# Optimization experiments

Measured on AMD Instinct MI355X. Metric: run time of the kernel, lower is better.

## Reference

```python
import jax, jax.numpy as jnp
import numpy as np

WINDOW = 256   # init kwarg window_size
CAUSAL = False # init kwarg causal


def setup_inputs() -> dict:
    key = jax.random.key(0)
    k1, k2, k3 = jax.random.split(key, 3)
    shape = (2, 16, 4096, 64)  # (batch, heads, seq_len, head_dim); seq_len % WINDOW == 0
    return {
        "query": jax.random.normal(k1, shape, dtype=jnp.float32),
        "key": jax.random.normal(k2, shape, dtype=jnp.float32),
        "value": jax.random.normal(k3, shape, dtype=jnp.float32),
    }


def _neighbor_blocks(x, nb, W):
    # x: [B,H,S,D] -> [B,H,nb,3W,D] where block n holds key blocks n-1,n,n+1 (zero padded at ends)
    B, H, S, D = x.shape
    xb = x.reshape(B, H, nb, W, D)
    xp = jnp.pad(xb, ((0, 0), (0, 0), (1, 1), (0, 0), (0, 0)))
    return jnp.concatenate([xp[:, :, j:j + nb] for j in range(3)], axis=3)


def _swa(query, key, value, window, causal):
    B, H, S, D = query.shape
    W = window
    nb = S // W
    scale = jnp.float32(1.0 / np.sqrt(D))
    qb = query.reshape(B, H, nb, W, D)
    kb = _neighbor_blocks(key, nb, W)    # [B,H,nb,3W,D]
    vb = _neighbor_blocks(value, nb, W)  # [B,H,nb,3W,D]

    # band mask: query global pos qi = n*W + q, key global pos ki = n*W + (k - W)
    qpos = jnp.arange(W)[:, None]              # [W,1]
    kpos = jnp.arange(3 * W)[None, :] - W      # [1,3W] relative block offset
    diff = kpos - qpos                         # [W,3W] == ki - qi
    ki = jnp.arange(nb)[:, None, None] * W + kpos[None]  # [nb,1,3W]
    valid = (ki >= 0) & (ki < S)
    if causal:
        band = (diff >= -W) & (diff <= 0)
    else:
        band = jnp.abs(diff) <= W
    mask = valid & band[None]                  # [nb,W,3W]

    scores = jnp.einsum('bhnqd,bhnkd->bhnqk', qb, kb) * scale  # [B,H,nb,W,3W]
    scores = jnp.where(mask, scores, -jnp.inf)
    attn = jax.nn.softmax(scores, axis=-1)
    out = jnp.einsum('bhnqk,bhnkd->bhnqd', attn, vb)
    return out.reshape(B, H, S, D)


def reference(query, key, value):
    return _swa(query, key, value, WINDOW, CAUSAL)
```

## Files before the change

kernel.cpp:

```cpp
#include <hip/hip_runtime.h>
#include <hip/hip_bf16.h>

typedef __attribute__((ext_vector_type(4)))  float f32x4;
typedef __attribute__((ext_vector_type(16))) float f32x16;
typedef __attribute__((ext_vector_type(8)))  short bf16x8;
typedef __attribute__((ext_vector_type(4)))  unsigned u32x4;

#define S_LEN 4096
#define HEAD_D 64
#define WIN 256
#define QBLK 128
#define KVBLK 64
#define KSTR 72
#define VSTR 72
#define QSCALE 0.18033688f

#define KBYTES (KVBLK * KSTR * 2)
#define VBYTES (HEAD_D * VSTR * 2)
#define KHALF  (KBYTES / 2)
#define VHALF  (VBYTES / 2)
#define LPAR_OFF (2 * KBYTES + 2 * VBYTES)
#define SMEM_BYTES (LPAR_OFF + 2 * 4 * 32 * 4)

static __device__ __forceinline__ unsigned cvt2(float lo, float hi) {
  unsigned r;
  asm("v_cvt_pk_bf16_f32 %0, %1, %2" : "=v"(r) : "v"(lo), "v"(hi));
  return r;
}

#define PUB_BARRIER() do {                              \
    __builtin_amdgcn_sched_barrier(0);                  \
    asm volatile("s_waitcnt lgkmcnt(0)" ::: "memory");  \
    __builtin_amdgcn_s_barrier();                       \
    __builtin_amdgcn_sched_barrier(0);                  \
  } while (0)

__global__ __launch_bounds__(512, 4)
void swa_fwd(const float* __restrict__ Q, const float* __restrict__ K,
             const float* __restrict__ V, float* __restrict__ O) {
  __shared__ __attribute__((aligned(16))) char smem[SMEM_BYTES];

  const int tid  = threadIdx.x;
  const int widx = tid >> 6;
  const int lane = tid & 63;
  const int hi   = lane >> 5;
  const int c    = lane & 31;
  const int qg   = widx & 3;
  const int kh   = widx >> 2;
  const int kho  = kh * 32;

  const int pb  = blockIdx.x;
  const int bh  = (pb & 7) * 4 + ((pb >> 3) >> 5);
  const int qb  = (pb >> 3) & 31;
  const int bq0 = qb * QBLK;
  const int q0w = bq0 + qg * 32;

  const size_t base = (size_t)bh * S_LEN * HEAD_D;
  const float* Qp = Q + base;
  const float* Kp = K + base;
  const float* Vp = V + base;
  float*       Op = O + base;

  const f32x16 Z16 = {0.f,0.f,0.f,0.f,0.f,0.f,0.f,0.f,0.f,0.f,0.f,0.f,0.f,0.f,0.f,0.f};

  bf16x8 aq[4];
  {
    const float* qr = Qp + (size_t)(q0w + c) * HEAD_D + hi * 8;
    #pragma unroll
    for (int ch = 0; ch < 4; ++ch) {
      f32x4 x0 = *(const f32x4*)(qr + ch * 16);
      f32x4 x1 = *(const f32x4*)(qr + ch * 16 + 4);
      u32x4 au;
      au[0] = cvt2(x0[0] * QSCALE, x0[1] * QSCALE);
      au[1] = cvt2(x0[2] * QSCALE, x0[3] * QSCALE);
      au[2] = cvt2(x1[0] * QSCALE, x1[1] * QSCALE);
      au[3] = cvt2(x1[2] * QSCALE, x1[3] * QSCALE);
      aq[ch] = __builtin_bit_cast(bf16x8, au);
    }
  }

  f32x16 acc0 = Z16, acc1 = Z16;
  float lsA = 0.f, lsB = 0.f;

  const int lo   = max(0, bq0 - WIN);
  const int khiB = min(S_LEN, bq0 + QBLK + WIN);
  const int nt   = (khiB - lo) >> 6;

  const int krow  = tid >> 3;
  const int kc8   = (tid & 7) << 3;
  const int key2  = (tid & 31) << 1;
  const int key2p = (key2 & ~12) | ((key2 & 4) << 1) | ((key2 & 8) >> 1);
  const int vd4   = (tid >> 5) << 2;

  short* const ksh = (short*)smem;
  short* const vsh = (short*)(smem + 2 * KBYTES);
  const short* const krd = ksh + (kho + c) * KSTR + hi * 8;
  const short* const vrd = vsh + c * VSTR + kho + hi * 8;
  short* const kwr = ksh + krow * KSTR + kc8;
  short* const vwr = vsh + vd4 * VSTR + key2p;

  unsigned koff = (unsigned)(lo + krow) * HEAD_D + kc8;
  unsigned voff = (unsigned)(lo + key2) * HEAD_D + vd4;

  f32x4 ka0, ka1, va0, va1;
  #define LOAD_TILE() do {                          \
    ka0 = *(const f32x4*)(Kp + koff);               \
    ka1 = *(const f32x4*)(Kp + koff + 4);           \
    va0 = *(const f32x4*)(Vp + voff);               \
    va1 = *(const f32x4*)(Vp + voff + HEAD_D);      \
    koff += KVBLK * HEAD_D;                         \
    voff += KVBLK * HEAD_D;                         \
  } while (0)

  #define STAGE_TO(BUF) do {                                        \
    u32x4 kw;                                                       \
    kw[0] = cvt2(ka0[0], ka0[1]);                                   \
    kw[1] = cvt2(ka0[2], ka0[3]);                                   \
    kw[2] = cvt2(ka1[0], ka1[1]);                                   \
    kw[3] = cvt2(ka1[2], ka1[3]);                                   \
    *(u32x4*)&kwr[(BUF) * KHALF] = kw;                              \
    _Pragma("unroll")                                               \
    for (int j = 0; j < 4; ++j)                                     \
      *(unsigned*)&vwr[(BUF) * VHALF + j * VSTR] = cvt2(va0[j], va1[j]); \
  } while (0)

  #define TILE_BODY(T, BUF) do {                                              \
    const int kv0_ = lo + ((T) << 6);                                         \
    f32x16 s = Z16;                                                           \
    __builtin_amdgcn_s_setprio(1);                                            \
    _Pragma("unroll")                                                         \
    for (int ch = 0; ch < 4; ++ch) {                                          \
      bf16x8 akf = *(const bf16x8*)&krd[(BUF) * KHALF + ch * 16];             \
      s = __builtin_amdgcn_mfma_f32_32x32x16_bf16(akf, aq[ch], s, 0, 0, 0);   \
    }                                                                         \
    __builtin_amdgcn_s_setprio(0);                                            \
    const int rel_ = kv0_ + kho - q0w;                                        \
    if (rel_ >= -224 && rel_ <= 224) {                                        \
      _Pragma("unroll")                                                       \
      for (int g = 0; g < 16; g += 2) {                                       \
        const float p0 = exp2f(s[g]);                                         \
        const float p1 = exp2f(s[g + 1]);                                     \
        s[g] = p0; s[g + 1] = p1; lsA += p0; lsB += p1;                       \
      }                                                                       \
    } else {                                                                  \
      const int bm_ = rel_ + 4 * hi - c + WIN;                                \
      _Pragma("unroll")                                                       \
      for (int g = 0; g < 16; ++g) {                                          \
        const int ro_ = (g & 3) + 8 * (g >> 2);                               \
        const float p = ((unsigned)(bm_ + ro_) <= 2u * WIN) ? exp2f(s[g]) : 0.f; \
        s[g] = p; if (g & 1) lsB += p; else lsA += p;                         \
      }                                                                       \
    }                                                                         \
    __builtin_amdgcn_s_setprio(1);                                            \
    _Pragma("unroll")                                                         \
    for (int kt = 0; kt < 2; ++kt) {                                          \
      u32x4 pau;                                                              \
      _Pragma("unroll")                                                       \
      for (int p2 = 0; p2 < 4; ++p2)                                          \
        pau[p2] = cvt2(s[kt * 8 + 2 * p2], s[kt * 8 + 2 * p2 + 1]);           \
      const bf16x8 pa = __builtin_bit_cast(bf16x8, pau);                      \
      bf16x8 bv0 = *(const bf16x8*)&vrd[(BUF) * VHALF + kt * 16];             \
      acc0 = __builtin_amdgcn_mfma_f32_32x32x16_bf16(pa, bv0, acc0, 0, 0, 0); \
      bf16x8 bv1 = *(const bf16x8*)&vrd[(BUF) * VHALF + kt * 16 + 32 * VSTR]; \
      acc1 = __builtin_amdgcn_mfma_f32_32x32x16_bf16(pa, bv1, acc1, 0, 0, 0); \
    }                                                                         \
    __builtin_amdgcn_s_setprio(0);                                            \
    if ((T) + 1 < nt) {                                                       \
      STAGE_TO((BUF) ^ 1);                                                    \
      if ((T) + 2 < nt) LOAD_TILE();                                          \
      PUB_BARRIER();                                                          \
    }                                                                         \
  } while (0)

  LOAD_TILE();
  STAGE_TO(0);
  LOAD_TILE();
  PUB_BARRIER();

  for (int t = 0; t < nt; t += 2) {
    TILE_BODY(t, 0);
    TILE_BODY(t + 1, 1);
  }

  float lsum = lsA + lsB;
  lsum += __shfl_xor(lsum, 32);
  __syncthreads();
  float* o_mrg = (float*)smem;
  float* l_par = (float*)(smem + LPAR_OFF);
  if (hi == 0) l_par[(kh * 4 + qg) * 32 + c] = lsum;
  if (kh == 0) {
    #pragma unroll
    for (int g = 0; g < 16; ++g) {
      const int qrow = (g & 3) + 8 * (g >> 2) + 4 * hi;
      o_mrg[(qg * 32 + qrow) * HEAD_D + c]      = acc0[g];
      o_mrg[(qg * 32 + qrow) * HEAD_D + 32 + c] = acc1[g];
    }
  }
  __syncthreads();
  if (kh == 1) {
    if (hi == 0) l_par[qg * 32 + c] = 1.0f / (l_par[qg * 32 + c] + l_par[(4 + qg) * 32 + c]);
    __asm__ volatile("s_waitcnt lgkmcnt(0)" ::: "memory");
    __builtin_amdgcn_sched_barrier(0);
    #pragma unroll
    for (int g = 0; g < 16; ++g) {
      const int qrow = (g & 3) + 8 * (g >> 2) + 4 * hi;
      const float iv = l_par[qg * 32 + qrow];
      float* orow = Op + (size_t)(q0w + qrow) * HEAD_D;
      orow[c]      = (o_mrg[(qg * 32 + qrow) * HEAD_D + c]      + acc0[g]) * iv;
      orow[32 + c] = (o_mrg[(qg * 32 + qrow) * HEAD_D + 32 + c] + acc1[g]) * iv;
    }
  }
}

extern "C" void kernel_launch(void* const* d_in, const int* in_sizes, int n_in,
                              void* d_out, int out_size, void* d_ws, size_t ws_size,
                              hipStream_t stream) {
  const float* q = (const float*)d_in[0];
  const float* k = (const float*)d_in[1];
  const float* v = (const float*)d_in[2];
  float* o = (float*)d_out;
  const int blocks = 2 * 16 * (S_LEN / QBLK);
  swa_fwd<<<dim3(blocks), dim3(512), 0, stream>>>(q, k, v, o);
}
```

Before: 51.25 us.

## Give each wave two query sets to reuse K/V fragments, halving block size

Workgroups shrink from 8 waves to 4. Each wave now handles two 32-row query sets that share every K and V fragment read from LDS, so each fragment feeds twice as many MFMAs. K and V global loads are split and issued between phases of the tile body, replacing the single next-tile prefetch, and exp2f becomes the raw hardware exp2 builtin. The cost is roughly double the accumulator and score registers per wave, fewer waves per block to hide latency, and a changed launch-bounds occupancy target.

```diff
diff --git a/kernel.cpp b/kernel.cpp
--- a/kernel.cpp
+++ b/kernel.cpp
@@ -20,7 +20,7 @@
 #define KHALF  (KBYTES / 2)
 #define VHALF  (VBYTES / 2)
 #define LPAR_OFF (2 * KBYTES + 2 * VBYTES)
-#define SMEM_BYTES (LPAR_OFF + 2 * 4 * 32 * 4)
+#define SMEM_BYTES (LPAR_OFF + 2 * 2 * 2 * 32 * 4)
 
 static __device__ __forceinline__ unsigned cvt2(float lo, float hi) {
   unsigned r;
@@ -35,25 +35,25 @@
     __builtin_amdgcn_sched_barrier(0);                  \
   } while (0)
 
-__global__ __launch_bounds__(512, 4)
+__global__ __launch_bounds__(256, 3)
 void swa_fwd(const float* __restrict__ Q, const float* __restrict__ K,
              const float* __restrict__ V, float* __restrict__ O) {
   __shared__ __attribute__((aligned(16))) char smem[SMEM_BYTES];
 
-  const int tid  = threadIdx.x;
-  const int widx = tid >> 6;
-  const int lane = tid & 63;
-  const int hi   = lane >> 5;
-  const int c    = lane & 31;
-  const int qg   = widx & 3;
-  const int kh   = widx >> 2;
-  const int kho  = kh * 32;
+  const int tid   = threadIdx.x;
+  const int widx  = tid >> 6;
+  const int lane  = tid & 63;
+  const int hi    = lane >> 5;
+  const int c     = lane & 31;
+  const int kh    = widx & 1;
+  const int qpair = widx >> 1;
+  const int kho   = kh * 32;
 
   const int pb  = blockIdx.x;
   const int bh  = (pb & 7) * 4 + ((pb >> 3) >> 5);
   const int qb  = (pb >> 3) & 31;
   const int bq0 = qb * QBLK;
-  const int q0w = bq0 + qg * 32;
+  const int q0  = bq0 + qpair * 64;
 
   const size_t base = (size_t)bh * S_LEN * HEAD_D;
   const float* Qp = Q + base;
@@ -63,9 +63,10 @@
 
   const f32x16 Z16 = {0.f,0.f,0.f,0.f,0.f,0.f,0.f,0.f,0.f,0.f,0.f,0.f,0.f,0.f,0.f,0.f};
 
-  bf16x8 aq[4];
-  {
-    const float* qr = Qp + (size_t)(q0w + c) * HEAD_D + hi * 8;
+  bf16x8 aqA[4], aqB[4];
+  #pragma unroll
+  for (int set = 0; set < 2; ++set) {
+    const float* qr = Qp + (size_t)(q0 + set * 32 + c) * HEAD_D + hi * 8;
     #pragma unroll
     for (int ch = 0; ch < 4; ++ch) {
       f32x4 x0 = *(const f32x4*)(qr + ch * 16);
@@ -75,106 +76,131 @@
       au[1] = cvt2(x0[2] * QSCALE, x0[3] * QSCALE);
       au[2] = cvt2(x1[0] * QSCALE, x1[1] * QSCALE);
       au[3] = cvt2(x1[2] * QSCALE, x1[3] * QSCALE);
-      aq[ch] = __builtin_bit_cast(bf16x8, au);
-    }
-  }
-
-  f32x16 acc0 = Z16, acc1 = Z16;
-  float lsA = 0.f, lsB = 0.f;
+      if (set == 0) aqA[ch] = __builtin_bit_cast(bf16x8, au);
+      else          aqB[ch] = __builtin_bit_cast(bf16x8, au);
+    }
+  }
+
+  f32x16 accA0 = Z16, accA1 = Z16, accB0 = Z16, accB1 = Z16;
+  float lsA0 = 0.f, lsA1 = 0.f, lsB0 = 0.f, lsB1 = 0.f;
 
   const int lo   = max(0, bq0 - WIN);
   const int khiB = min(S_LEN, bq0 + QBLK + WIN);
   const int nt   = (khiB - lo) >> 6;
 
-  const int krow  = tid >> 3;
-  const int kc8   = (tid & 7) << 3;
+  const int krow  = tid >> 2;
+  const int kc16  = (tid & 3) << 4;
   const int key2  = (tid & 31) << 1;
   const int key2p = (key2 & ~12) | ((key2 & 4) << 1) | ((key2 & 8) >> 1);
-  const int vd4   = (tid >> 5) << 2;
+  const int vd8   = (tid >> 5) << 3;
 
   short* const ksh = (short*)smem;
   short* const vsh = (short*)(smem + 2 * KBYTES);
   const short* const krd = ksh + (kho + c) * KSTR + hi * 8;
   const short* const vrd = vsh + c * VSTR + kho + hi * 8;
-  short* const kwr = ksh + krow * KSTR + kc8;
-  short* const vwr = vsh + vd4 * VSTR + key2p;
-
-  unsigned koff = (unsigned)(lo + krow) * HEAD_D + kc8;
-  unsigned voff = (unsigned)(lo + key2) * HEAD_D + vd4;
-
-  f32x4 ka0, ka1, va0, va1;
-  #define LOAD_TILE() do {                          \
-    ka0 = *(const f32x4*)(Kp + koff);               \
-    ka1 = *(const f32x4*)(Kp + koff + 4);           \
-    va0 = *(const f32x4*)(Vp + voff);               \
-    va1 = *(const f32x4*)(Vp + voff + HEAD_D);      \
-    koff += KVBLK * HEAD_D;                         \
-    voff += KVBLK * HEAD_D;                         \
-  } while (0)
-
+  short* const kwr = ksh + krow * KSTR + kc16;
+  short* const vwr = vsh + vd8 * VSTR + key2p;
+
+  unsigned koff = (unsigned)(lo + krow) * HEAD_D + kc16;
+  unsigned voff = (unsigned)(lo + key2) * HEAD_D + vd8;
+
+  f32x4 k0, k1, k2, k3;
+  f32x4 v00, v01, v10, v11;
+  #define LOAD_K() do {                         \
+    k0 = *(const f32x4*)(Kp + koff);            \
+    k1 = *(const f32x4*)(Kp + koff + 4);        \
+    k2 = *(const f32x4*)(Kp + koff + 8);        \
+    k3 = *(const f32x4*)(Kp + koff + 12);       \
+    koff += KVBLK * HEAD_D;                     \
+  } while (0)
+  #define LOAD_V() do {                         \
+    v00 = *(const f32x4*)(Vp + voff);           \
+    v01 = *(const f32x4*)(Vp + voff + 4);       \
+    v10 = *(const f32x4*)(Vp + voff + HEAD_D);  \
+    v11 = *(const f32x4*)(Vp + voff + HEAD_D + 4); \
+    voff += KVBLK * HEAD_D;                     \
+  } while (0)
   #define STAGE_TO(BUF) do {                                        \
     u32x4 kw;                                                       \
-    kw[0] = cvt2(ka0[0], ka0[1]);                                   \
-    kw[1] = cvt2(ka0[2], ka0[3]);                                   \
-    kw[2] = cvt2(ka1[0], ka1[1]);                                   \
-    kw[3] = cvt2(ka1[2], ka1[3]);                                   \
+    kw[0] = cvt2(k0[0], k0[1]);  kw[1] = cvt2(k0[2], k0[3]);        \
+    kw[2] = cvt2(k1[0], k1[1]);  kw[3] = cvt2(k1[2], k1[3]);        \
     *(u32x4*)&kwr[(BUF) * KHALF] = kw;                              \
+    kw[0] = cvt2(k2[0], k2[1]);  kw[1] = cvt2(k2[2], k2[3]);        \
+    kw[2] = cvt2(k3[0], k3[1]);  kw[3] = cvt2(k3[2], k3[3]);        \
+    *(u32x4*)&kwr[(BUF) * KHALF + 8] = kw;                          \
     _Pragma("unroll")                                               \
     for (int j = 0; j < 4; ++j)                                     \
-      *(unsigned*)&vwr[(BUF) * VHALF + j * VSTR] = cvt2(va0[j], va1[j]); \
-  } while (0)
-
-  #define TILE_BODY(T, BUF) do {                                              \
-    const int kv0_ = lo + ((T) << 6);                                         \
-    f32x16 s = Z16;                                                           \
-    __builtin_amdgcn_s_setprio(1);                                            \
-    _Pragma("unroll")                                                         \
-    for (int ch = 0; ch < 4; ++ch) {                                          \
-      bf16x8 akf = *(const bf16x8*)&krd[(BUF) * KHALF + ch * 16];             \
-      s = __builtin_amdgcn_mfma_f32_32x32x16_bf16(akf, aq[ch], s, 0, 0, 0);   \
-    }                                                                         \
-    __builtin_amdgcn_s_setprio(0);                                            \
-    const int rel_ = kv0_ + kho - q0w;                                        \
-    if (rel_ >= -224 && rel_ <= 224) {                                        \
-      _Pragma("unroll")                                                       \
-      for (int g = 0; g < 16; g += 2) {                                       \
-        const float p0 = exp2f(s[g]);                                         \
-        const float p1 = exp2f(s[g + 1]);                                     \
-        s[g] = p0; s[g + 1] = p1; lsA += p0; lsB += p1;                       \
-      }                                                                       \
-    } else {                                                                  \
-      const int bm_ = rel_ + 4 * hi - c + WIN;                                \
-      _Pragma("unroll")                                                       \
-      for (int g = 0; g < 16; ++g) {                                          \
-        const int ro_ = (g & 3) + 8 * (g >> 2);                               \
-        const float p = ((unsigned)(bm_ + ro_) <= 2u * WIN) ? exp2f(s[g]) : 0.f; \
-        s[g] = p; if (g & 1) lsB += p; else lsA += p;                         \
-      }                                                                       \
-    }                                                                         \
-    __builtin_amdgcn_s_setprio(1);                                            \
-    _Pragma("unroll")                                                         \
-    for (int kt = 0; kt < 2; ++kt) {                                          \
-      u32x4 pau;                                                              \
-      _Pragma("unroll")                                                       \
-      for (int p2 = 0; p2 < 4; ++p2)                                          \
-        pau[p2] = cvt2(s[kt * 8 + 2 * p2], s[kt * 8 + 2 * p2 + 1]);           \
-      const bf16x8 pa = __builtin_bit_cast(bf16x8, pau);                      \
-      bf16x8 bv0 = *(const bf16x8*)&vrd[(BUF) * VHALF + kt * 16];             \
-      acc0 = __builtin_amdgcn_mfma_f32_32x32x16_bf16(pa, bv0, acc0, 0, 0, 0); \
-      bf16x8 bv1 = *(const bf16x8*)&vrd[(BUF) * VHALF + kt * 16 + 32 * VSTR]; \
-      acc1 = __builtin_amdgcn_mfma_f32_32x32x16_bf16(pa, bv1, acc1, 0, 0, 0); \
-    }                                                                         \
-    __builtin_amdgcn_s_setprio(0);                                            \
-    if ((T) + 1 < nt) {                                                       \
-      STAGE_TO((BUF) ^ 1);                                                    \
-      if ((T) + 2 < nt) LOAD_TILE();                                          \
-      PUB_BARRIER();                                                          \
-    }                                                                         \
-  } while (0)
-
-  LOAD_TILE();
+      *(unsigned*)&vwr[(BUF) * VHALF + j * VSTR] = cvt2(v00[j], v10[j]); \
+    _Pragma("unroll")                                               \
+    for (int j = 0; j < 4; ++j)                                     \
+      *(unsigned*)&vwr[(BUF) * VHALF + (4 + j) * VSTR] = cvt2(v01[j], v11[j]); \
+  } while (0)
+
+  #define TILE_BODY(T, BUF) do {                                                  \
+    const int rel_ = lo + ((T) << 6) + kho - q0;                                  \
+    f32x16 sA = Z16, sB = Z16;                                                    \
+    __builtin_amdgcn_s_setprio(1);                                                \
+    _Pragma("unroll")                                                             \
+    for (int ch = 0; ch < 4; ++ch) {                                              \
+      bf16x8 akf = *(const bf16x8*)&krd[(BUF) * KHALF + ch * 16];                 \
+      sA = __builtin_amdgcn_mfma_f32_32x32x16_bf16(akf, aqA[ch], sA, 0, 0, 0);    \
+      sB = __builtin_amdgcn_mfma_f32_32x32x16_bf16(akf, aqB[ch], sB, 0, 0, 0);    \
+    }                                                                             \
+    __builtin_amdgcn_s_setprio(0);                                                \
+    if ((T) + 1 < nt) LOAD_K();                                                   \
+    if (rel_ >= -192 && rel_ <= 224) {     \
+      _Pragma("unroll")                                                           \
+      for (int g = 0; g < 16; g += 2) {                                           \
+        const float a0 = __builtin_amdgcn_exp2f(sA[g]);                           \
+        const float a1 = __builtin_amdgcn_exp2f(sA[g + 1]);                       \
+        const float b0 = __builtin_amdgcn_exp2f(sB[g]);                           \
+        const float b1 = __builtin_amdgcn_exp2f(sB[g + 1]);                       \
+        sA[g] = a0; sA[g + 1] = a1; sB[g] = b0; sB[g + 1] = b1;                   \
+        lsA0 += a0; lsA1 += a1; lsB0 += b0; lsB1 += b1;                           \
+      }                                                                           \
+    } else {                                                                      \
+      const int bmA = rel_ + 4 * hi - c + WIN;                                    \
+      _Pragma("unroll")                                                           \
+      for (int g = 0; g < 16; ++g) {                                              \
+        const int ro_ = (g & 3) + 8 * (g >> 2);                                   \
+        const float a = ((unsigned)(bmA + ro_) <= 2u * WIN)                       \
+                          ? __builtin_amdgcn_exp2f(sA[g]) : 0.f;                  \
+        const float b = ((unsigned)(bmA - 32 + ro_) <= 2u * WIN)                  \
+                          ? __builtin_amdgcn_exp2f(sB[g]) : 0.f;                  \
+        sA[g] = a; sB[g] = b;                                                     \
+        if (g & 1) { lsA1 += a; lsB1 += b; } else { lsA0 += a; lsB0 += b; }       \
+      }                                                                           \
+    }                                                                             \
+    if ((T) + 1 < nt) LOAD_V();                                                   \
+    __builtin_amdgcn_s_setprio(1);                                                \
+    _Pragma("unroll")                                                             \
+    for (int kt = 0; kt < 2; ++kt) {                                              \
+      u32x4 pau;                                                                  \
+      _Pragma("unroll")                                                           \
+      for (int p2 = 0; p2 < 4; ++p2)                                              \
+        pau[p2] = cvt2(sA[kt * 8 + 2 * p2], sA[kt * 8 + 2 * p2 + 1]);             \
+      const bf16x8 paA = __builtin_bit_cast(bf16x8, pau);                         \
+      _Pragma("unroll")                                                           \
+      for (int p2 = 0; p2 < 4; ++p2)                                              \
+        pau[p2] = cvt2(sB[kt * 8 + 2 * p2], sB[kt * 8 + 2 * p2 + 1]);             \
+      const bf16x8 paB = __builtin_bit_cast(bf16x8, pau);                         \
+      bf16x8 bv0 = *(const bf16x8*)&vrd[(BUF) * VHALF + kt * 16];                 \
+      accA0 = __builtin_amdgcn_mfma_f32_32x32x16_bf16(paA, bv0, accA0, 0, 0, 0);  \
+      accB0 = __builtin_amdgcn_mfma_f32_32x32x16_bf16(paB, bv0, accB0, 0, 0, 0);  \
+      bf16x8 bv1 = *(const bf16x8*)&vrd[(BUF) * VHALF + kt * 16 + 32 * VSTR];     \
+      accA1 = __builtin_amdgcn_mfma_f32_32x32x16_bf16(paA, bv1, accA1, 0, 0, 0);  \
+      accB1 = __builtin_amdgcn_mfma_f32_32x32x16_bf16(paB, bv1, accB1, 0, 0, 0);  \
+    }                                                                             \
+    __builtin_amdgcn_s_setprio(0);                                                \
+    if ((T) + 1 < nt) {                                                           \
+      STAGE_TO((BUF) ^ 1);                                                        \
+      PUB_BARRIER();                                                              \
+    }                                                                             \
+  } while (0)
+
+  LOAD_K();
+  LOAD_V();
   STAGE_TO(0);
-  LOAD_TILE();
   PUB_BARRIER();
 
   for (int t = 0; t < nt; t += 2) {
@@ -182,32 +208,48 @@
     TILE_BODY(t + 1, 1);
   }
 
-  float lsum = lsA + lsB;
-  lsum += __shfl_xor(lsum, 32);
+  float lsA = lsA0 + lsA1;  lsA += __shfl_xor(lsA, 32);
+  float lsB = lsB0 + lsB1;  lsB += __shfl_xor(lsB, 32);
   __syncthreads();
   float* o_mrg = (float*)smem;
   float* l_par = (float*)(smem + LPAR_OFF);
-  if (hi == 0) l_par[(kh * 4 + qg) * 32 + c] = lsum;
+  if (hi == 0) {
+    l_par[(((kh * 2 + qpair) * 2 + 0) * 32) + c] = lsA;
+    l_par[(((kh * 2 + qpair) * 2 + 1) * 32) + c] = lsB;
+  }
   if (kh == 0) {
+    float* om = o_mrg + (size_t)qpair * 64 * HEAD_D;
     #pragma unroll
     for (int g = 0; g < 16; ++g) {
       const int qrow = (g & 3) + 8 * (g >> 2) + 4 * hi;
-      o_mrg[(qg * 32 + qrow) * HEAD_D + c]      = acc0[g];
-      o_mrg[(qg * 32 + qrow) * HEAD_D + 32 + c] = acc1[g];
+      om[qrow * HEAD_D + c]             = accA0[g];
+      om[qrow * HEAD_D + 32 + c]        = accA1[g];
+      om[(32 + qrow) * HEAD_D + c]      = accB0[g];
+      om[(32 + qrow) * HEAD_D + 32 + c] = accB1[g];
     }
   }
   __syncthreads();
   if (kh == 1) {
-    if (hi == 0) l_par[qg * 32 + c] = 1.0f / (l_par[qg * 32 + c] + l_par[(4 + qg) * 32 + c]);
+    float* lp = l_par + qpair * 2 * 32;
+    const float* lp1 = lp + 2 * 2 * 32 * 1;
+    if (hi == 0) {
+      lp[c]      = 1.0f / (lp[c]      + lp1[c]);
+      lp[32 + c] = 1.0f / (lp[32 + c] + lp1[32 + c]);
+    }
     __asm__ volatile("s_waitcnt lgkmcnt(0)" ::: "memory");
     __builtin_amdgcn_sched_barrier(0);
+    const float* om = o_mrg + (size_t)qpair * 64 * HEAD_D;
     #pragma unroll
     for (int g = 0; g < 16; ++g) {
       const int qrow = (g & 3) + 8 * (g >> 2) + 4 * hi;
-      const float iv = l_par[qg * 32 + qrow];
-      float* orow = Op + (size_t)(q0w + qrow) * HEAD_D;
-      orow[c]      = (o_mrg[(qg * 32 + qrow) * HEAD_D + c]      + acc0[g]) * iv;
-      orow[32 + c] = (o_mrg[(qg * 32 + qrow) * HEAD_D + 32 + c] + acc1[g]) * iv;
+      const float ivA = lp[qrow];
+      const float ivB = lp[32 + qrow];
+      float* orA = Op + (size_t)(q0 + qrow) * HEAD_D;
+      float* orB = Op + (size_t)(q0 + 32 + qrow) * HEAD_D;
+      orA[c]      = (om[qrow * HEAD_D + c]             + accA0[g]) * ivA;
+      orA[32 + c] = (om[qrow * HEAD_D + 32 + c]        + accA1[g]) * ivA;
+      orB[c]      = (om[(32 + qrow) * HEAD_D + c]      + accB0[g]) * ivB;
+      orB[32 + c] = (om[(32 + qrow) * HEAD_D + 32 + c] + accB1[g]) * ivB;
     }
   }
 }
@@ -220,5 +262,5 @@
   const float* v = (const float*)d_in[2];
   float* o = (float*)d_out;
   const int blocks = 2 * 16 * (S_LEN / QBLK);
-  swa_fwd<<<dim3(blocks), dim3(512), 0, stream>>>(q, k, v, o);
+  swa_fwd<<<dim3(blocks), dim3(256), 0, stream>>>(q, k, v, o);
 }
```

Result: slower. 149.7 us (+192.0%).

## Double query block to 256 rows with 16 waves and skip dead KV tiles

Applied to the files above, without the earlier changes.

Grows each workgroup to 256 query rows and 1024 threads, so each staged K/V tile is shared by more query waves and the redundant halo reloads per block drop. Splits global loads so half the waves load K and half load V. Waves whose 32-key slice lies outside the band skip the MFMA and softmax work but still stage and hit the barrier. Also switches to the hardware exp2 intrinsic and does the output merge in two phases to fit shared memory. In exchange, fewer but larger blocks run, which may reduce occupancy, and barrier waits involve more waves.

```diff
diff --git a/kernel.cpp b/kernel.cpp
--- a/kernel.cpp
+++ b/kernel.cpp
@@ -9,7 +9,7 @@
 #define S_LEN 4096
 #define HEAD_D 64
 #define WIN 256
-#define QBLK 128
+#define QBLK 256
 #define KVBLK 64
 #define KSTR 72
 #define VSTR 72
@@ -20,7 +20,7 @@
 #define KHALF  (KBYTES / 2)
 #define VHALF  (VBYTES / 2)
 #define LPAR_OFF (2 * KBYTES + 2 * VBYTES)
-#define SMEM_BYTES (LPAR_OFF + 2 * 4 * 32 * 4)
+#define SMEM_BYTES (LPAR_OFF + 2 * 8 * 32 * 4)
 
 static __device__ __forceinline__ unsigned cvt2(float lo, float hi) {
   unsigned r;
@@ -35,7 +35,7 @@
     __builtin_amdgcn_sched_barrier(0);                  \
   } while (0)
 
-__global__ __launch_bounds__(512, 4)
+__global__ __launch_bounds__(1024, 4)
 void swa_fwd(const float* __restrict__ Q, const float* __restrict__ K,
              const float* __restrict__ V, float* __restrict__ O) {
   __shared__ __attribute__((aligned(16))) char smem[SMEM_BYTES];
@@ -45,15 +45,15 @@
   const int lane = tid & 63;
   const int hi   = lane >> 5;
   const int c    = lane & 31;
-  const int qg   = widx & 3;
-  const int kh   = widx >> 2;
+  const int kh   = widx & 1;
+  const int qg   = widx >> 1;
   const int kho  = kh * 32;
 
   const int pb  = blockIdx.x;
-  const int bh  = (pb & 7) * 4 + ((pb >> 3) >> 5);
-  const int qb  = (pb >> 3) & 31;
+  const int bh  = (pb & 7) * 4 + ((pb >> 3) >> 4);
+  const int qb  = (pb >> 3) & 15;
   const int bq0 = qb * QBLK;
-  const int q0w = bq0 + qg * 32;
+  const int q0  = bq0 + qg * 32;
 
   const size_t base = (size_t)bh * S_LEN * HEAD_D;
   const float* Qp = Q + base;
@@ -65,7 +65,7 @@
 
   bf16x8 aq[4];
   {
-    const float* qr = Qp + (size_t)(q0w + c) * HEAD_D + hi * 8;
+    const float* qr = Qp + (size_t)(q0 + c) * HEAD_D + hi * 8;
     #pragma unroll
     for (int ch = 0; ch < 4; ++ch) {
       f32x4 x0 = *(const f32x4*)(qr + ch * 16);
@@ -86,90 +86,107 @@
   const int khiB = min(S_LEN, bq0 + QBLK + WIN);
   const int nt   = (khiB - lo) >> 6;
 
-  const int krow  = tid >> 3;
-  const int kc8   = (tid & 7) << 3;
-  const int key2  = (tid & 31) << 1;
+  const bool isK = (widx < 8);
+  const int vtid  = tid & 511;
+  const int key2  = (vtid & 31) << 1;
   const int key2p = (key2 & ~12) | ((key2 & 4) << 1) | ((key2 & 8) >> 1);
-  const int vd4   = (tid >> 5) << 2;
+  const int vd4   = (vtid >> 5) << 2;
 
   short* const ksh = (short*)smem;
   short* const vsh = (short*)(smem + 2 * KBYTES);
   const short* const krd = ksh + (kho + c) * KSTR + hi * 8;
   const short* const vrd = vsh + c * VSTR + kho + hi * 8;
-  short* const kwr = ksh + krow * KSTR + kc8;
-  short* const vwr = vsh + vd4 * VSTR + key2p;
-
-  unsigned koff = (unsigned)(lo + krow) * HEAD_D + kc8;
-  unsigned voff = (unsigned)(lo + key2) * HEAD_D + vd4;
-
-  f32x4 ka0, ka1, va0, va1;
-  #define LOAD_TILE() do {                          \
-    ka0 = *(const f32x4*)(Kp + koff);               \
-    ka1 = *(const f32x4*)(Kp + koff + 4);           \
-    va0 = *(const f32x4*)(Vp + voff);               \
-    va1 = *(const f32x4*)(Vp + voff + HEAD_D);      \
-    koff += KVBLK * HEAD_D;                         \
-    voff += KVBLK * HEAD_D;                         \
-  } while (0)
-
-  #define STAGE_TO(BUF) do {                                        \
-    u32x4 kw;                                                       \
-    kw[0] = cvt2(ka0[0], ka0[1]);                                   \
-    kw[1] = cvt2(ka0[2], ka0[3]);                                   \
-    kw[2] = cvt2(ka1[0], ka1[1]);                                   \
-    kw[3] = cvt2(ka1[2], ka1[3]);                                   \
-    *(u32x4*)&kwr[(BUF) * KHALF] = kw;                              \
-    _Pragma("unroll")                                               \
-    for (int j = 0; j < 4; ++j)                                     \
-      *(unsigned*)&vwr[(BUF) * VHALF + j * VSTR] = cvt2(va0[j], va1[j]); \
-  } while (0)
-
-  #define TILE_BODY(T, BUF) do {                                              \
-    const int kv0_ = lo + ((T) << 6);                                         \
-    f32x16 s = Z16;                                                           \
-    __builtin_amdgcn_s_setprio(1);                                            \
-    _Pragma("unroll")                                                         \
-    for (int ch = 0; ch < 4; ++ch) {                                          \
-      bf16x8 akf = *(const bf16x8*)&krd[(BUF) * KHALF + ch * 16];             \
-      s = __builtin_amdgcn_mfma_f32_32x32x16_bf16(akf, aq[ch], s, 0, 0, 0);   \
-    }                                                                         \
-    __builtin_amdgcn_s_setprio(0);                                            \
-    const int rel_ = kv0_ + kho - q0w;                                        \
-    if (rel_ >= -224 && rel_ <= 224) {                                        \
-      _Pragma("unroll")                                                       \
-      for (int g = 0; g < 16; g += 2) {                                       \
-        const float p0 = exp2f(s[g]);                                         \
-        const float p1 = exp2f(s[g + 1]);                                     \
-        s[g] = p0; s[g + 1] = p1; lsA += p0; lsB += p1;                       \
-      }                                                                       \
-    } else {                                                                  \
-      const int bm_ = rel_ + 4 * hi - c + WIN;                                \
-      _Pragma("unroll")                                                       \
-      for (int g = 0; g < 16; ++g) {                                          \
-        const int ro_ = (g & 3) + 8 * (g >> 2);                               \
-        const float p = ((unsigned)(bm_ + ro_) <= 2u * WIN) ? exp2f(s[g]) : 0.f; \
-        s[g] = p; if (g & 1) lsB += p; else lsA += p;                         \
-      }                                                                       \
-    }                                                                         \
-    __builtin_amdgcn_s_setprio(1);                                            \
-    _Pragma("unroll")                                                         \
-    for (int kt = 0; kt < 2; ++kt) {                                          \
-      u32x4 pau;                                                              \
-      _Pragma("unroll")                                                       \
-      for (int p2 = 0; p2 < 4; ++p2)                                          \
-        pau[p2] = cvt2(s[kt * 8 + 2 * p2], s[kt * 8 + 2 * p2 + 1]);           \
-      const bf16x8 pa = __builtin_bit_cast(bf16x8, pau);                      \
-      bf16x8 bv0 = *(const bf16x8*)&vrd[(BUF) * VHALF + kt * 16];             \
-      acc0 = __builtin_amdgcn_mfma_f32_32x32x16_bf16(pa, bv0, acc0, 0, 0, 0); \
-      bf16x8 bv1 = *(const bf16x8*)&vrd[(BUF) * VHALF + kt * 16 + 32 * VSTR]; \
-      acc1 = __builtin_amdgcn_mfma_f32_32x32x16_bf16(pa, bv1, acc1, 0, 0, 0); \
-    }                                                                         \
-    __builtin_amdgcn_s_setprio(0);                                            \
-    if ((T) + 1 < nt) {                                                       \
-      STAGE_TO((BUF) ^ 1);                                                    \
-      if ((T) + 2 < nt) LOAD_TILE();                                          \
-      PUB_BARRIER();                                                          \
-    }                                                                         \
+
+  const float* src;
+  unsigned off;
+  int off2;
+  short* swr;
+  if (isK) {
+    src  = Kp;
+    off  = (unsigned)(lo + (vtid >> 3)) * HEAD_D + ((vtid & 7) << 3);
+    off2 = 4;
+    swr  = ksh + (vtid >> 3) * KSTR + ((vtid & 7) << 3);
+  } else {
+    src  = Vp;
+    off  = (unsigned)(lo + key2) * HEAD_D + vd4;
+    off2 = HEAD_D;
+    swr  = vsh + vd4 * VSTR + key2p;
+  }
+
+  f32x4 r0, r1;
+  #define LOAD_TILE() do {                       \
+    r0 = *(const f32x4*)(src + off);             \
+    r1 = *(const f32x4*)(src + off + off2);      \
+    off += KVBLK * HEAD_D;                       \
+  } while (0)
+
+  #define STAGE_TO(BUF) do {                                          \
+    if (isK) {                                                        \
+      u32x4 kw;                                                       \
+      kw[0] = cvt2(r0[0], r0[1]);  kw[1] = cvt2(r0[2], r0[3]);        \
+      kw[2] = cvt2(r1[0], r1[1]);  kw[3] = cvt2(r1[2], r1[3]);        \
+      *(u32x4*)&swr[(BUF) * KHALF] = kw;                              \
+    } else {                                                          \
+      _Pragma("unroll")                                               \
+      for (int j = 0; j < 4; ++j)                                     \
+        *(unsigned*)&swr[(BUF) * VHALF + j * VSTR] = cvt2(r0[j], r1[j]); \
+    }                                                                 \
+  } while (0)
+
+  #define TILE_BODY(T, BUF) do {                                                  \
+    const int rel_ = lo + ((T) << 6) + kho - q0;                                  \
+    const bool live_ = (rel_ >= -287) && (rel_ <= 287);   \
+    if (live_) {                                                                  \
+      f32x16 s = Z16;                                                             \
+      __builtin_amdgcn_s_setprio(1);                                              \
+      _Pragma("unroll")                                                           \
+      for (int ch = 0; ch < 4; ++ch) {                                            \
+        bf16x8 akf = *(const bf16x8*)&krd[(BUF) * KHALF + ch * 16];               \
+        s = __builtin_amdgcn_mfma_f32_32x32x16_bf16(akf, aq[ch], s, 0, 0, 0);     \
+      }                                                                           \
+      __builtin_amdgcn_s_setprio(0);                                              \
+      if ((T) + 1 < nt) {                                                         \
+        STAGE_TO((BUF) ^ 1);                                                      \
+        if ((T) + 2 < nt) LOAD_TILE();                                            \
+      }                                                                           \
+      if (rel_ >= -224 && rel_ <= 224) {              \
+        _Pragma("unroll")                                                         \
+        for (int g = 0; g < 16; g += 2) {                                         \
+          const float p0 = __builtin_amdgcn_exp2f(s[g]);                          \
+          const float p1 = __builtin_amdgcn_exp2f(s[g + 1]);                      \
+          s[g] = p0; s[g + 1] = p1; lsA += p0; lsB += p1;                         \
+        }                                                                         \
+      } else {                                                                    \
+        const int bm_ = rel_ + 4 * hi - c + WIN;                                  \
+        _Pragma("unroll")                                                         \
+        for (int g = 0; g < 16; ++g) {                                            \
+          const int ro_ = (g & 3) + 8 * (g >> 2);                                 \
+          const float p = ((unsigned)(bm_ + ro_) <= 2u * WIN)                     \
+                            ? __builtin_amdgcn_exp2f(s[g]) : 0.f;                 \
+          s[g] = p; if (g & 1) lsB += p; else lsA += p;                           \
+        }                                                                         \
+      }                                                                           \
+      __builtin_amdgcn_s_setprio(1);                                              \
+      _Pragma("unroll")                                                           \
+      for (int kt = 0; kt < 2; ++kt) {                                            \
+        u32x4 pau;                                                                \
+        _Pragma("unroll")                                                         \
+        for (int p2 = 0; p2 < 4; ++p2)                                            \
+          pau[p2] = cvt2(s[kt * 8 + 2 * p2], s[kt * 8 + 2 * p2 + 1]);             \
+        const bf16x8 pa = __builtin_bit_cast(bf16x8, pau);                        \
+        bf16x8 bv0 = *(const bf16x8*)&vrd[(BUF) * VHALF + kt * 16];               \
+        acc0 = __builtin_amdgcn_mfma_f32_32x32x16_bf16(pa, bv0, acc0, 0, 0, 0);   \
+        bf16x8 bv1 = *(const bf16x8*)&vrd[(BUF) * VHALF + kt * 16 + 32 * VSTR];   \
+        acc1 = __builtin_amdgcn_mfma_f32_32x32x16_bf16(pa, bv1, acc1, 0, 0, 0);   \
+      }                                                                           \
+      __builtin_amdgcn_s_setprio(0);                                              \
+    } else {                                                                      \
+      if ((T) + 1 < nt) {                                                         \
+        STAGE_TO((BUF) ^ 1);                                                      \
+        if ((T) + 2 < nt) LOAD_TILE();                                            \
+      }                                                                           \
+    }                                                                             \
+    if ((T) + 1 < nt) PUB_BARRIER();                                              \
   } while (0)
 
   LOAD_TILE();
@@ -184,30 +201,38 @@
 
   float lsum = lsA + lsB;
   lsum += __shfl_xor(lsum, 32);
-  __syncthreads();
   float* o_mrg = (float*)smem;
   float* l_par = (float*)(smem + LPAR_OFF);
-  if (hi == 0) l_par[(kh * 4 + qg) * 32 + c] = lsum;
-  if (kh == 0) {
-    #pragma unroll
-    for (int g = 0; g < 16; ++g) {
-      const int qrow = (g & 3) + 8 * (g >> 2) + 4 * hi;
-      o_mrg[(qg * 32 + qrow) * HEAD_D + c]      = acc0[g];
-      o_mrg[(qg * 32 + qrow) * HEAD_D + 32 + c] = acc1[g];
+  __syncthreads();
+  if (hi == 0) l_par[(kh * 8 + qg) * 32 + c] = lsum;
+  #pragma unroll
+  for (int p = 0; p < 2; ++p) {
+    if (p) __syncthreads();
+    if (kh == 0 && (qg >> 2) == p) {
+      float* om = o_mrg + (qg & 3) * 32 * HEAD_D;
+      #pragma unroll
+      for (int g = 0; g < 16; ++g) {
+        const int qrow = (g & 3) + 8 * (g >> 2) + 4 * hi;
+        om[qrow * HEAD_D + c]      = acc0[g];
+        om[qrow * HEAD_D + 32 + c] = acc1[g];
+      }
     }
-  }
-  __syncthreads();
-  if (kh == 1) {
-    if (hi == 0) l_par[qg * 32 + c] = 1.0f / (l_par[qg * 32 + c] + l_par[(4 + qg) * 32 + c]);
-    __asm__ volatile("s_waitcnt lgkmcnt(0)" ::: "memory");
-    __builtin_amdgcn_sched_barrier(0);
-    #pragma unroll
-    for (int g = 0; g < 16; ++g) {
-      const int qrow = (g & 3) + 8 * (g >> 2) + 4 * hi;
-      const float iv = l_par[qg * 32 + qrow];
-      float* orow = Op + (size_t)(q0w + qrow) * HEAD_D;
-      orow[c]      = (o_mrg[(qg * 32 + qrow) * HEAD_D + c]      + acc0[g]) * iv;
-      orow[32 + c] = (o_mrg[(qg * 32 + qrow) * HEAD_D + 32 + c] + acc1[g]) * iv;
+    __syncthreads();
+    if (kh == 1 && (qg >> 2) == p) {
+      float* lp = l_par + qg * 32;
+      const float* lp1 = l_par + (8 + qg) * 32;
+      if (hi == 0) lp[c] = 1.0f / (lp[c] + lp1[c]);
+      __asm__ volatile("s_waitcnt lgkmcnt(0)" ::: "memory");
+      __builtin_amdgcn_sched_barrier(0);
+      const float* om = o_mrg + (qg & 3) * 32 * HEAD_D;
+      #pragma unroll
+      for (int g = 0; g < 16; ++g) {
+        const int qrow = (g & 3) + 8 * (g >> 2) + 4 * hi;
+        const float iv = lp[qrow];
+        float* orow = Op + (size_t)(q0 + qrow) * HEAD_D;
+        orow[c]      = (om[qrow * HEAD_D + c]      + acc0[g]) * iv;
+        orow[32 + c] = (om[qrow * HEAD_D + 32 + c] + acc1[g]) * iv;
+      }
     }
   }
 }
@@ -220,5 +245,5 @@
   const float* v = (const float*)d_in[2];
   float* o = (float*)d_out;
   const int blocks = 2 * 16 * (S_LEN / QBLK);
-  swa_fwd<<<dim3(blocks), dim3(512), 0, stream>>>(q, k, v, o);
+  swa_fwd<<<dim3(blocks), dim3(1024), 0, stream>>>(q, k, v, o);
 }
```

Measured after the change: 48.17 us. 1.06x faster.
